# Performance work log

Measured on AMD Instinct MI355X. Metric: run time of the kernel, lower is better.

The kernel has to match this reference:

```python
import jax, jax.numpy as jnp
import numpy as np

B, N, V, H, Z = 2048, 32, 10, 256, 64


def setup_inputs() -> dict:
    key = jax.random.key(0)
    ks = jax.random.split(key, 14)
    # strictly upper-triangular random DAG adjacency (topological order = vertex index)
    p = jax.random.uniform(ks[0], (B, N, N))
    tri = jnp.triu(jnp.ones((N, N), jnp.float32), k=1)
    adj = (p < 0.12).astype(jnp.float32) * tri
    node_types = jax.random.randint(ks[1], (B, N), 0, V).astype(jnp.int32)
    s = 0.05
    return dict(
        adj=adj,
        node_types=node_types,
        w_ih=jax.random.normal(ks[2], (V, 3 * H), jnp.float32) * s,
        w_hh=jax.random.normal(ks[3], (H, 3 * H), jnp.float32) * s,
        b_ih=jax.random.normal(ks[4], (3 * H,), jnp.float32) * s,
        b_hh=jax.random.normal(ks[5], (3 * H,), jnp.float32) * s,
        w_gate=jax.random.normal(ks[6], (H, H), jnp.float32) * s,
        b_gate=jax.random.normal(ks[7], (H,), jnp.float32) * s,
        w_map=jax.random.normal(ks[8], (H, H), jnp.float32) * s,
        w_mu=jax.random.normal(ks[9], (H, Z), jnp.float32) * s,
        b_mu=jax.random.normal(ks[10], (Z,), jnp.float32) * s,
        w_std=jax.random.normal(ks[11], (H, Z), jnp.float32) * s,
        b_std=jax.random.normal(ks[12], (Z,), jnp.float32) * s,
    )


def _gru_cell(x, h, w_ih, w_hh, b_ih, b_hh):
    # torch GRUCell math; weights stored [in, 3H]
    gi = x @ w_ih + b_ih  # [B, 3H]
    gh = h @ w_hh + b_hh
    i_r, i_z, i_n = jnp.split(gi, 3, axis=-1)
    h_r, h_z, h_n = jnp.split(gh, 3, axis=-1)
    r = jax.nn.sigmoid(i_r + h_r)
    z = jax.nn.sigmoid(i_z + h_z)
    n = jnp.tanh(i_n + r * h_n)
    return (1.0 - z) * n + z * h


def reference(adj, node_types, w_ih, w_hh, b_ih, b_hh, w_gate, b_gate, w_map,
              w_mu, b_mu, w_std, b_std):
    x_all = jax.nn.one_hot(node_types, V, dtype=adj.dtype)  # [B, N, V]
    hidden0 = jnp.zeros((B, N, H), adj.dtype)
    adj_cols = jnp.transpose(adj, (2, 0, 1))  # [N, B, N]; col v = predecessor mask of v
    x_seq = jnp.transpose(x_all, (1, 0, 2))   # [N, B, V]

    def step(hidden, inps):
        col, x, v = inps
        # gate(h_pred) * map(h_pred), summed over predecessors. map has no bias,
        # so non-predecessor (zero-masked) rows contribute exactly zero, matching
        # the padded-gather formulation in the original code.
        gm = jax.nn.sigmoid(hidden @ w_gate + b_gate) * (hidden @ w_map)  # [B, N, H]
        agg = jnp.einsum('bn,bnh->bh', col, gm)  # [B, H]; zero for v=0 (no preds)
        h_new = _gru_cell(x, agg, w_ih, w_hh, b_ih, b_hh)  # [B, H]
        hidden = jax.lax.dynamic_update_slice(hidden, h_new[:, None, :], (0, v, 0))
        return hidden, None

    hidden, _ = jax.lax.scan(step, hidden0, (adj_cols, x_seq, jnp.arange(N)))
    hg = hidden[:, -1, :]  # graph state = last vertex hidden
    mu = hg @ w_mu + b_mu
    sigma = hg @ w_std + b_std
    return (mu, sigma)
```

## Files before the change

### kernel.cpp

```cpp
#include <hip/hip_runtime.h>


#define BB 2048
#define NN 32
#define VV 10
#define HH 256
#define ZZ 64
#define BT 8
#define KC 8
#define NT1 48
#define NT2 32
#define WHH_ELEMS (NT1 * KC * 64 * 8)
#define WGM_ELEMS (NT2 * KC * 64 * 8)
#define GM_BYTE_OFF ((WHH_ELEMS + WGM_ELEMS) * 2)
#define SLAB_ELEMS (BT * NN * HH)
#define SLAB_BYTES (SLAB_ELEMS * 2)

typedef __attribute__((ext_vector_type(8))) short frag8;
typedef __attribute__((ext_vector_type(4))) float facc4;
typedef __attribute__((ext_vector_type(4))) unsigned short us4;

__device__ __forceinline__ float bf2f(unsigned short u) {
    unsigned int x = ((unsigned int)u) << 16;
    return __builtin_bit_cast(float, x);
}
__device__ __forceinline__ unsigned short f2bf(float f) {
    unsigned int x = __builtin_bit_cast(unsigned int, f);
    x += 0x7FFFu + ((x >> 16) & 1u);
    return (unsigned short)(x >> 16);
}
__device__ __forceinline__ float sigm(float x) { return 1.0f / (1.0f + __expf(-x)); }
__device__ __forceinline__ float ldv(const float* p, size_t i) { return p[i]; }
__device__ __forceinline__ float ldv(const unsigned short* p, size_t i) { return bf2f(p[i]); }
__device__ __forceinline__ void stv(float* p, size_t i, float v) { p[i] = v; }
__device__ __forceinline__ void stv(unsigned short* p, size_t i, float v) { p[i] = f2bf(v); }
__device__ __forceinline__ us4 ntld4(const unsigned short* p) {
    return __builtin_nontemporal_load((const us4*)p);
}
__device__ __forceinline__ void ntst(unsigned short* p, unsigned short v) {
    __builtin_nontemporal_store(v, p);
}

__global__ void detect_dtype(const unsigned short* __restrict__ w, int* flag) {
    __shared__ int zc, bc;
    if (threadIdx.x == 0) { zc = 0; bc = 0; }
    __syncthreads();
    int z = 0, b = 0;
    for (int i = threadIdx.x; i < 2048; i += 256) {
        unsigned short lo = w[2 * i];
        if (lo == 0) z++;
        unsigned e = (lo >> 7) & 0xFFu;
        if (e >= 0x86u) b++;
    }
    atomicAdd(&zc, z); atomicAdd(&bc, b);
    __syncthreads();
    if (threadIdx.x == 0) *flag = (bc > 0 || zc > 512) ? 1 : 0;
}

template <typename T>
__global__ void repack_weights(const T* __restrict__ w_hh,
                               const T* __restrict__ w_gate,
                               const T* __restrict__ w_map,
                               unsigned short* __restrict__ whh_p,
                               unsigned short* __restrict__ wgm_p,
                               const int* __restrict__ flag, int want) {
    if (*flag != want) return;
    int t = blockIdx.x * blockDim.x + threadIdx.x;
    int lane = t & 63;
    int frag = t >> 6;
    int kbase = (lane >> 4) * 8;
    if (frag < NT1 * KC) {
        int jt = frag / KC, kc = frag % KC;
        int col = jt * 16 + (lane & 15);
        unsigned short* dst = whh_p + ((size_t)frag * 64 + lane) * 8;
        #pragma unroll
        for (int j = 0; j < 8; ++j)
            dst[j] = f2bf(ldv(w_hh, (size_t)(kc * 32 + kbase + j) * 768 + col));
    } else if (frag < (NT1 + NT2) * KC) {
        int f2 = frag - NT1 * KC;
        int jt = f2 / KC, kc = f2 % KC;
        int col = jt * 16 + (lane & 15);
        unsigned short* dst = wgm_p + ((size_t)f2 * 64 + lane) * 8;
        #pragma unroll
        for (int j = 0; j < 8; ++j) {
            int k = kc * 32 + kbase + j;
            dst[j] = f2bf((col < HH) ? ldv(w_gate, (size_t)k * HH + col)
                                     : ldv(w_map, (size_t)k * HH + (col - HH)));
        }
    }
}

template <typename T>
__global__ __launch_bounds__(1024, 4) void vae_main(
    const T* __restrict__ adj,
    const int* __restrict__ ntypes,
    const T* __restrict__ w_ih,
    const T* __restrict__ b_ih,
    const T* __restrict__ b_hh,
    const T* __restrict__ b_gate,
    const T* __restrict__ w_mu,
    const T* __restrict__ b_mu,
    const T* __restrict__ w_std,
    const T* __restrict__ b_std,
    const unsigned short* __restrict__ whh_p,
    const unsigned short* __restrict__ wgm_p,
    unsigned short* __restrict__ gm_base,
    T* __restrict__ out,
    int b_start,
    const int* __restrict__ flag, int want)
{
    if (*flag != want) return;

    __shared__ __align__(16) float agg[BT][HH];
    __shared__ __align__(16) unsigned short aggbf[16][264];
    __shared__ __align__(16) unsigned short hnew[16][264];
    __shared__ unsigned int  amask[BT][NN];
    __shared__ int           ntva[BT][NN];
    __shared__ __align__(16) unsigned short wihL[VV * 776];
    __shared__ __align__(16) float bihL[768], bhhL[768], bgL[HH];

    const int tid  = threadIdx.x;
    const int lane = tid & 63;
    const int w    = tid >> 6;
    const int b0   = b_start + blockIdx.x * BT;

    unsigned short* gms = gm_base + (size_t)blockIdx.x * SLAB_ELEMS;

    const frag8* whh8 = (const frag8*)whh_p;
    const frag8* wgm8 = (const frag8*)wgm_p;

    for (int i = 8 * 264 + tid; i < 16 * 264; i += 1024) {
        ((unsigned short*)aggbf)[i] = 0;
        ((unsigned short*)hnew)[i]  = 0;
    }
    if (tid < 256) {
        int bi = tid >> 5, vv = tid & 31;
        unsigned m = 0;
        for (int n = 0; n < NN; ++n)
            if (ldv(adj, ((size_t)(b0 + bi) * NN + n) * NN + vv) != 0.0f) m |= (1u << n);
        amask[bi][vv] = m;
    } else if (tid < 512) {
        int idx = tid - 256;
        int bi = idx >> 5, vv = idx & 31;
        ntva[bi][vv] = ntypes[(b0 + bi) * NN + vv];
    }
    for (int i = tid; i < VV * 768; i += 1024) {
        int r = i / 768, c = i - r * 768;
        wihL[r * 776 + c] = f2bf(ldv(w_ih, (size_t)i));
    }
    for (int i = tid; i < 768; i += 1024) { bihL[i] = ldv(b_ih, i); bhhL[i] = ldv(b_hh, i); }
    if (tid < HH) bgL[tid] = ldv(b_gate, tid);
    __syncthreads();

    for (int v = 0; v < NN; ++v) {
        if (w < BT) {
            const int bi = w;
            const int h4 = lane * 4;
            unsigned m = amask[bi][v];
            float a0 = 0.f, a1 = 0.f, a2 = 0.f, a3 = 0.f;
            const unsigned short* rb = gms + (size_t)bi * NN * HH + h4;
            while (m) {
                int n = __builtin_ctz(m); m &= m - 1;
                us4 g = ntld4(rb + (size_t)n * HH);
                a0 += bf2f(g.x); a1 += bf2f(g.y); a2 += bf2f(g.z); a3 += bf2f(g.w);
            }
            *(float4*)&agg[bi][h4] = make_float4(a0, a1, a2, a3);
            ushort4 ab; ab.x = f2bf(a0); ab.y = f2bf(a1); ab.z = f2bf(a2); ab.w = f2bf(a3);
            *(ushort4*)&aggbf[bi][h4] = ab;
        }
        __syncthreads();

        {
            frag8 afrag[KC];
            #pragma unroll
            for (int kc = 0; kc < KC; ++kc)
                afrag[kc] = *(const frag8*)&aggbf[lane & 15][kc * 32 + (lane >> 4) * 8];

            const int t = w;
            facc4 aR = {0.f, 0.f, 0.f, 0.f};
            facc4 aZ = {0.f, 0.f, 0.f, 0.f};
            facc4 aN = {0.f, 0.f, 0.f, 0.f};
            const frag8* pR = whh8 + (size_t)(t     ) * (KC * 64) + lane;
            const frag8* pZ = whh8 + (size_t)(t + 16) * (KC * 64) + lane;
            const frag8* pN = whh8 + (size_t)(t + 32) * (KC * 64) + lane;
            #pragma unroll
            for (int kc = 0; kc < KC; ++kc) {
                aR = __builtin_amdgcn_mfma_f32_16x16x32_bf16(afrag[kc], pR[kc * 64], aR, 0, 0, 0);
                aZ = __builtin_amdgcn_mfma_f32_16x16x32_bf16(afrag[kc], pZ[kc * 64], aZ, 0, 0, 0);
                aN = __builtin_amdgcn_mfma_f32_16x16x32_bf16(afrag[kc], pN[kc * 64], aN, 0, 0, 0);
            }
            const int col = t * 16 + (lane & 15);
            const int q = lane >> 4;
            if (q < 2) {
                const float bir  = bihL[col],       bhr = bhhL[col];
                const float biz  = bihL[col + 256], bhz = bhhL[col + 256];
                const float bin_ = bihL[col + 512], bhn = bhhL[col + 512];
                #pragma unroll
                for (int i = 0; i < 4; ++i) {
                    const int bi = 4 * q + i;
                    const int ty = ntva[bi][v] * 776;
                    const float xr = bf2f(wihL[ty + col]);
                    const float xz = bf2f(wihL[ty + col + 256]);
                    const float xn = bf2f(wihL[ty + col + 512]);
                    const float r = sigm(xr + bir + aR[i] + bhr);
                    const float z = sigm(xz + biz + aZ[i] + bhz);
                    const float n = tanhf(xn + bin_ + r * (aN[i] + bhn));
                    const float h = (1.f - z) * n + z * agg[bi][col];
                    hnew[bi][col] = f2bf(h);
                }
            }
        }
        __syncthreads();

        {
            frag8 hfrag[KC];
            #pragma unroll
            for (int kc = 0; kc < KC; ++kc)
                hfrag[kc] = *(const frag8*)&hnew[lane & 15][kc * 32 + (lane >> 4) * 8];

            const int t = w;
            facc4 aG = {0.f, 0.f, 0.f, 0.f};
            facc4 aM = {0.f, 0.f, 0.f, 0.f};
            const frag8* pG = wgm8 + (size_t)(t     ) * (KC * 64) + lane;
            const frag8* pM = wgm8 + (size_t)(t + 16) * (KC * 64) + lane;
            #pragma unroll
            for (int kc = 0; kc < KC; ++kc) {
                aG = __builtin_amdgcn_mfma_f32_16x16x32_bf16(hfrag[kc], pG[kc * 64], aG, 0, 0, 0);
                aM = __builtin_amdgcn_mfma_f32_16x16x32_bf16(hfrag[kc], pM[kc * 64], aM, 0, 0, 0);
            }
            const int col = t * 16 + (lane & 15);
            const int q = lane >> 4;
            if (q < 2) {
                const float bg = bgL[col];
                #pragma unroll
                for (int i = 0; i < 4; ++i) {
                    const int bi = 4 * q + i;
                    const float gv = sigm(aG[i] + bg) * aM[i];
                    ntst(gms + (size_t)(bi * NN + v) * HH + col, f2bf(gv));
                }
            }
        }
        __syncthreads();
    }

    {
        const int bi = w >> 1, half = w & 1, z = lane;
        float am = 0.f, as = 0.f;
        const int h0 = half * 128;
        #pragma unroll 4
        for (int h = h0; h < h0 + 128; ++h) {
            const float hv = bf2f(hnew[bi][h]);
            am += hv * ldv(w_mu, (size_t)h * ZZ + z);
            as += hv * ldv(w_std, (size_t)h * ZZ + z);
        }
        agg[bi][half * 64 + z]       = am;
        agg[bi][128 + half * 64 + z] = as;
    }
    __syncthreads();
    if (w < BT) {
        const int bi = w, z = lane;
        const float am = agg[bi][z] + agg[bi][64 + z] + ldv(b_mu, z);
        const float as = agg[bi][128 + z] + agg[bi][192 + z] + ldv(b_std, z);
        stv(out, (size_t)(b0 + bi) * ZZ + z, am);
        stv(out, (size_t)BB * ZZ + (size_t)(b0 + bi) * ZZ + z, as);
    }
}

extern "C" void kernel_launch(void* const* d_in, const int* in_sizes, int n_in,
                              void* d_out, int out_size, void* d_ws, size_t ws_size,
                              hipStream_t stream)
{
    unsigned short* whh_p = (unsigned short*)d_ws;
    unsigned short* wgm_p = whh_p + WHH_ELEMS;
    unsigned short* gm_base = wgm_p + WGM_ELEMS;

    size_t flag_off = (ws_size >= 8) ? ((ws_size - 4) & ~(size_t)3) : 0;
    int* flag = (int*)((char*)d_ws + flag_off);

    long long avail = (long long)flag_off - (long long)GM_BYTE_OFF;
    int cb = (int)(avail / SLAB_BYTES);
    if (cb < 1) cb = 1;
    if (cb > BB / BT) cb = BB / BT;

    detect_dtype<<<dim3(1), 256, 0, stream>>>((const unsigned short*)d_in[2], flag);

    repack_weights<float><<<dim3(160), 256, 0, stream>>>(
        (const float*)d_in[3], (const float*)d_in[6], (const float*)d_in[8],
        whh_p, wgm_p, flag, 1);
    repack_weights<unsigned short><<<dim3(160), 256, 0, stream>>>(
        (const unsigned short*)d_in[3], (const unsigned short*)d_in[6],
        (const unsigned short*)d_in[8], whh_p, wgm_p, flag, 0);

    const int nblk = BB / BT;
    for (int blk0 = 0; blk0 < nblk; blk0 += cb) {
        int g = nblk - blk0; if (g > cb) g = cb;
        vae_main<float><<<dim3(g), 1024, 0, stream>>>(
            (const float*)d_in[0], (const int*)d_in[1], (const float*)d_in[2],
            (const float*)d_in[4], (const float*)d_in[5], (const float*)d_in[7],
            (const float*)d_in[9], (const float*)d_in[10], (const float*)d_in[11],
            (const float*)d_in[12],
            whh_p, wgm_p, gm_base, (float*)d_out, blk0 * BT, flag, 1);
        vae_main<unsigned short><<<dim3(g), 1024, 0, stream>>>(
            (const unsigned short*)d_in[0], (const int*)d_in[1],
            (const unsigned short*)d_in[2], (const unsigned short*)d_in[4],
            (const unsigned short*)d_in[5], (const unsigned short*)d_in[7],
            (const unsigned short*)d_in[9], (const unsigned short*)d_in[10],
            (const unsigned short*)d_in[11], (const unsigned short*)d_in[12],
            whh_p, wgm_p, gm_base, (unsigned short*)d_out, blk0 * BT, flag, 0);
    }
}
```

Measured before the change: 580.5 us.

## Stage gate*map rows in LDS and write back coalesced; keep gate weights in registers

Instead of each thread issuing scattered 2-byte nontemporal stores of the gate*map row to the global slab, the row is written to a shared-memory buffer. Spare waves then flush it to global memory with 16-byte stores during the next step's aggregation. The immediately preceding vertex's contribution is read straight from LDS rather than from global memory. The gate weight fragments are also preloaded into registers once, removing repeated global loads in the inner MFMA loop, at the cost of extra VGPR pressure and another LDS buffer.

```diff
diff --git a/kernel.cpp b/kernel.cpp
--- a/kernel.cpp
+++ b/kernel.cpp
@@ -19,6 +19,7 @@
 typedef __attribute__((ext_vector_type(8))) short frag8;
 typedef __attribute__((ext_vector_type(4))) float facc4;
 typedef __attribute__((ext_vector_type(4))) unsigned short us4;
+typedef __attribute__((ext_vector_type(8))) unsigned short us8;
 
 __device__ __forceinline__ float bf2f(unsigned short u) {
     unsigned int x = ((unsigned int)u) << 16;
@@ -37,8 +38,8 @@
 __device__ __forceinline__ us4 ntld4(const unsigned short* p) {
     return __builtin_nontemporal_load((const us4*)p);
 }
-__device__ __forceinline__ void ntst(unsigned short* p, unsigned short v) {
-    __builtin_nontemporal_store(v, p);
+__device__ __forceinline__ void ntst16(unsigned short* p, us8 v) {
+    __builtin_nontemporal_store(v, (us8*)p);
 }
 
 __global__ void detect_dtype(const unsigned short* __restrict__ w, int* flag) {
@@ -114,6 +115,7 @@
     __shared__ __align__(16) float agg[BT][HH];
     __shared__ __align__(16) unsigned short aggbf[16][264];
     __shared__ __align__(16) unsigned short hnew[16][264];
+    __shared__ __align__(16) unsigned short gmrow[BT][HH];
     __shared__ unsigned int  amask[BT][NN];
     __shared__ int           ntva[BT][NN];
     __shared__ __align__(16) unsigned short wihL[VV * 776];
@@ -150,13 +152,21 @@
     }
     for (int i = tid; i < 768; i += 1024) { bihL[i] = ldv(b_ih, i); bhhL[i] = ldv(b_hh, i); }
     if (tid < HH) bgL[tid] = ldv(b_gate, tid);
+
+    frag8 wG[KC];
+    {
+        const frag8* pG = wgm8 + (size_t)w * (KC * 64) + lane;
+        #pragma unroll
+        for (int kc = 0; kc < KC; ++kc) wG[kc] = pG[kc * 64];
+    }
     __syncthreads();
 
     for (int v = 0; v < NN; ++v) {
         if (w < BT) {
             const int bi = w;
             const int h4 = lane * 4;
-            unsigned m = amask[bi][v];
+            unsigned m0 = amask[bi][v];
+            unsigned m  = (v > 0) ? (m0 & ~(1u << (v - 1))) : m0;
             float a0 = 0.f, a1 = 0.f, a2 = 0.f, a3 = 0.f;
             const unsigned short* rb = gms + (size_t)bi * NN * HH + h4;
             while (m) {
@@ -164,9 +174,19 @@
                 us4 g = ntld4(rb + (size_t)n * HH);
                 a0 += bf2f(g.x); a1 += bf2f(g.y); a2 += bf2f(g.z); a3 += bf2f(g.w);
             }
+            if (v > 0 && ((m0 >> (v - 1)) & 1u)) {
+                const unsigned short* gr = &gmrow[bi][h4];
+                a0 += bf2f(gr[0]); a1 += bf2f(gr[1]);
+                a2 += bf2f(gr[2]); a3 += bf2f(gr[3]);
+            }
             *(float4*)&agg[bi][h4] = make_float4(a0, a1, a2, a3);
             ushort4 ab; ab.x = f2bf(a0); ab.y = f2bf(a1); ab.z = f2bf(a2); ab.w = f2bf(a3);
             *(ushort4*)&aggbf[bi][h4] = ab;
+        } else if (w < 12 && v > 0) {
+            const int bi = (w - 8) * 2 + (lane >> 5);
+            const int c8 = (lane & 31) * 8;
+            us8 val = *(const us8*)&gmrow[bi][c8];
+            ntst16(gms + ((size_t)bi * NN + (v - 1)) * HH + c8, val);
         }
         __syncthreads();
 
@@ -221,11 +241,10 @@
             const int t = w;
             facc4 aG = {0.f, 0.f, 0.f, 0.f};
             facc4 aM = {0.f, 0.f, 0.f, 0.f};
-            const frag8* pG = wgm8 + (size_t)(t     ) * (KC * 64) + lane;
             const frag8* pM = wgm8 + (size_t)(t + 16) * (KC * 64) + lane;
             #pragma unroll
             for (int kc = 0; kc < KC; ++kc) {
-                aG = __builtin_amdgcn_mfma_f32_16x16x32_bf16(hfrag[kc], pG[kc * 64], aG, 0, 0, 0);
+                aG = __builtin_amdgcn_mfma_f32_16x16x32_bf16(hfrag[kc], wG[kc], aG, 0, 0, 0);
                 aM = __builtin_amdgcn_mfma_f32_16x16x32_bf16(hfrag[kc], pM[kc * 64], aM, 0, 0, 0);
             }
             const int col = t * 16 + (lane & 15);
@@ -235,8 +254,7 @@
                 #pragma unroll
                 for (int i = 0; i < 4; ++i) {
                     const int bi = 4 * q + i;
-                    const float gv = sigm(aG[i] + bg) * aM[i];
-                    ntst(gms + (size_t)(bi * NN + v) * HH + col, f2bf(gv));
+                    gmrow[bi][col] = f2bf(sigm(aG[i] + bg) * aM[i]);
                 }
             }
         }
```

Result: faster. 559.0 us (-3.7%).

## Keep per-block gate*map history in LDS instead of global workspace slab

Applied to the files above, without the earlier changes.

Moves the per-graph gm history (8 graphs x 32 nodes x 256 bf16, 128KB) from a global workspace slab into dynamic shared memory, so the per-step aggregation reads and writes stay on-chip. This also removes the chunked multi-launch loop. To make room, it shrinks the padded aggbf/hnew buffers, stores biases as bf16, and drops the LDS copy of w_ih in favour of direct global reads. It also keeps the R and G weight fragments in registers across steps. The large LDS footprint allows only one block per CU and adds register pressure, but it removes the global memory round-trips that sat on the serial dependency chain.

```diff
diff --git a/kernel.cpp b/kernel.cpp
--- a/kernel.cpp
+++ b/kernel.cpp
@@ -12,13 +12,10 @@
 #define NT2 32
 #define WHH_ELEMS (NT1 * KC * 64 * 8)
 #define WGM_ELEMS (NT2 * KC * 64 * 8)
-#define GM_BYTE_OFF ((WHH_ELEMS + WGM_ELEMS) * 2)
-#define SLAB_ELEMS (BT * NN * HH)
-#define SLAB_BYTES (SLAB_ELEMS * 2)
+#define DYN_LDS_BYTES (BT * NN * HH * 2)
 
 typedef __attribute__((ext_vector_type(8))) short frag8;
 typedef __attribute__((ext_vector_type(4))) float facc4;
-typedef __attribute__((ext_vector_type(4))) unsigned short us4;
 
 __device__ __forceinline__ float bf2f(unsigned short u) {
     unsigned int x = ((unsigned int)u) << 16;
@@ -34,12 +31,6 @@
 __device__ __forceinline__ float ldv(const unsigned short* p, size_t i) { return bf2f(p[i]); }
 __device__ __forceinline__ void stv(float* p, size_t i, float v) { p[i] = v; }
 __device__ __forceinline__ void stv(unsigned short* p, size_t i, float v) { p[i] = f2bf(v); }
-__device__ __forceinline__ us4 ntld4(const unsigned short* p) {
-    return __builtin_nontemporal_load((const us4*)p);
-}
-__device__ __forceinline__ void ntst(unsigned short* p, unsigned short v) {
-    __builtin_nontemporal_store(v, p);
-}
 
 __global__ void detect_dtype(const unsigned short* __restrict__ w, int* flag) {
     __shared__ int zc, bc;
@@ -104,35 +95,29 @@
     const T* __restrict__ b_std,
     const unsigned short* __restrict__ whh_p,
     const unsigned short* __restrict__ wgm_p,
-    unsigned short* __restrict__ gm_base,
     T* __restrict__ out,
-    int b_start,
     const int* __restrict__ flag, int want)
 {
     if (*flag != want) return;
 
+    extern __shared__ __align__(16) char dyn_lds[];
+    unsigned short* gmS = (unsigned short*)dyn_lds;
+
     __shared__ __align__(16) float agg[BT][HH];
-    __shared__ __align__(16) unsigned short aggbf[16][264];
-    __shared__ __align__(16) unsigned short hnew[16][264];
+    __shared__ __align__(16) unsigned short aggbf[BT][264];
+    __shared__ __align__(16) unsigned short hnew[BT][264];
     __shared__ unsigned int  amask[BT][NN];
     __shared__ int           ntva[BT][NN];
-    __shared__ __align__(16) unsigned short wihL[VV * 776];
-    __shared__ __align__(16) float bihL[768], bhhL[768], bgL[HH];
+    __shared__ unsigned short bihL[768], bhhL[768], bgL[HH];
 
     const int tid  = threadIdx.x;
     const int lane = tid & 63;
     const int w    = tid >> 6;
-    const int b0   = b_start + blockIdx.x * BT;
-
-    unsigned short* gms = gm_base + (size_t)blockIdx.x * SLAB_ELEMS;
+    const int b0   = blockIdx.x * BT;
 
     const frag8* whh8 = (const frag8*)whh_p;
     const frag8* wgm8 = (const frag8*)wgm_p;
 
-    for (int i = 8 * 264 + tid; i < 16 * 264; i += 1024) {
-        ((unsigned short*)aggbf)[i] = 0;
-        ((unsigned short*)hnew)[i]  = 0;
-    }
     if (tid < 256) {
         int bi = tid >> 5, vv = tid & 31;
         unsigned m = 0;
@@ -144,26 +129,45 @@
         int bi = idx >> 5, vv = idx & 31;
         ntva[bi][vv] = ntypes[(b0 + bi) * NN + vv];
     }
-    for (int i = tid; i < VV * 768; i += 1024) {
-        int r = i / 768, c = i - r * 768;
-        wihL[r * 776 + c] = f2bf(ldv(w_ih, (size_t)i));
-    }
-    for (int i = tid; i < 768; i += 1024) { bihL[i] = ldv(b_ih, i); bhhL[i] = ldv(b_hh, i); }
-    if (tid < HH) bgL[tid] = ldv(b_gate, tid);
+    for (int i = tid; i < 768; i += 1024) {
+        bihL[i] = f2bf(ldv(b_ih, i));
+        bhhL[i] = f2bf(ldv(b_hh, i));
+    }
+    if (tid < HH) bgL[tid] = f2bf(ldv(b_gate, tid));
+
+    frag8 wR[KC], wG[KC];
+    {
+        const frag8* pR = whh8 + (size_t)w * (KC * 64) + lane;
+        const frag8* pG = wgm8 + (size_t)w * (KC * 64) + lane;
+        #pragma unroll
+        for (int kc = 0; kc < KC; ++kc) { wR[kc] = pR[kc * 64]; wG[kc] = pG[kc * 64]; }
+    }
     __syncthreads();
+
+    const int arow  = lane & 15;
+    const int acol0 = (lane >> 4) * 8;
 
     for (int v = 0; v < NN; ++v) {
         if (w < BT) {
             const int bi = w;
             const int h4 = lane * 4;
+            const unsigned short* rb = gmS + (size_t)(bi * NN) * HH + h4;
             unsigned m = amask[bi][v];
             float a0 = 0.f, a1 = 0.f, a2 = 0.f, a3 = 0.f;
-            const unsigned short* rb = gms + (size_t)bi * NN * HH + h4;
+            float c0 = 0.f, c1 = 0.f, c2 = 0.f, c3 = 0.f;
             while (m) {
-                int n = __builtin_ctz(m); m &= m - 1;
-                us4 g = ntld4(rb + (size_t)n * HH);
-                a0 += bf2f(g.x); a1 += bf2f(g.y); a2 += bf2f(g.z); a3 += bf2f(g.w);
-            }
+                int n0 = __builtin_ctz(m); m &= m - 1;
+                const ushort4 g0 = *(const ushort4*)(rb + n0 * HH);
+                if (m) {
+                    int n1 = __builtin_ctz(m); m &= m - 1;
+                    const ushort4 g1 = *(const ushort4*)(rb + n1 * HH);
+                    c0 += bf2f(g1.x); c1 += bf2f(g1.y);
+                    c2 += bf2f(g1.z); c3 += bf2f(g1.w);
+                }
+                a0 += bf2f(g0.x); a1 += bf2f(g0.y);
+                a2 += bf2f(g0.z); a3 += bf2f(g0.w);
+            }
+            a0 += c0; a1 += c1; a2 += c2; a3 += c3;
             *(float4*)&agg[bi][h4] = make_float4(a0, a1, a2, a3);
             ushort4 ab; ab.x = f2bf(a0); ab.y = f2bf(a1); ab.z = f2bf(a2); ab.w = f2bf(a3);
             *(ushort4*)&aggbf[bi][h4] = ab;
@@ -172,36 +176,40 @@
 
         {
             frag8 afrag[KC];
-            #pragma unroll
-            for (int kc = 0; kc < KC; ++kc)
-                afrag[kc] = *(const frag8*)&aggbf[lane & 15][kc * 32 + (lane >> 4) * 8];
+            if (arow < BT) {
+                #pragma unroll
+                for (int kc = 0; kc < KC; ++kc)
+                    afrag[kc] = *(const frag8*)&aggbf[arow][kc * 32 + acol0];
+            } else {
+                #pragma unroll
+                for (int kc = 0; kc < KC; ++kc) afrag[kc] = frag8{};
+            }
 
             const int t = w;
             facc4 aR = {0.f, 0.f, 0.f, 0.f};
             facc4 aZ = {0.f, 0.f, 0.f, 0.f};
             facc4 aN = {0.f, 0.f, 0.f, 0.f};
-            const frag8* pR = whh8 + (size_t)(t     ) * (KC * 64) + lane;
             const frag8* pZ = whh8 + (size_t)(t + 16) * (KC * 64) + lane;
             const frag8* pN = whh8 + (size_t)(t + 32) * (KC * 64) + lane;
             #pragma unroll
             for (int kc = 0; kc < KC; ++kc) {
-                aR = __builtin_amdgcn_mfma_f32_16x16x32_bf16(afrag[kc], pR[kc * 64], aR, 0, 0, 0);
+                aR = __builtin_amdgcn_mfma_f32_16x16x32_bf16(afrag[kc], wR[kc], aR, 0, 0, 0);
                 aZ = __builtin_amdgcn_mfma_f32_16x16x32_bf16(afrag[kc], pZ[kc * 64], aZ, 0, 0, 0);
                 aN = __builtin_amdgcn_mfma_f32_16x16x32_bf16(afrag[kc], pN[kc * 64], aN, 0, 0, 0);
             }
             const int col = t * 16 + (lane & 15);
             const int q = lane >> 4;
             if (q < 2) {
-                const float bir  = bihL[col],       bhr = bhhL[col];
-                const float biz  = bihL[col + 256], bhz = bhhL[col + 256];
-                const float bin_ = bihL[col + 512], bhn = bhhL[col + 512];
+                const float bir  = bf2f(bihL[col]),       bhr = bf2f(bhhL[col]);
+                const float biz  = bf2f(bihL[col + 256]), bhz = bf2f(bhhL[col + 256]);
+                const float bin_ = bf2f(bihL[col + 512]), bhn = bf2f(bhhL[col + 512]);
                 #pragma unroll
                 for (int i = 0; i < 4; ++i) {
                     const int bi = 4 * q + i;
-                    const int ty = ntva[bi][v] * 776;
-                    const float xr = bf2f(wihL[ty + col]);
-                    const float xz = bf2f(wihL[ty + col + 256]);
-                    const float xn = bf2f(wihL[ty + col + 512]);
+                    const size_t ty = (size_t)ntva[bi][v] * 768;
+                    const float xr = ldv(w_ih, ty + col);
+                    const float xz = ldv(w_ih, ty + col + 256);
+                    const float xn = ldv(w_ih, ty + col + 512);
                     const float r = sigm(xr + bir + aR[i] + bhr);
                     const float z = sigm(xz + biz + aZ[i] + bhz);
                     const float n = tanhf(xn + bin_ + r * (aN[i] + bhn));
@@ -214,29 +222,32 @@
 
         {
             frag8 hfrag[KC];
-            #pragma unroll
-            for (int kc = 0; kc < KC; ++kc)
-                hfrag[kc] = *(const frag8*)&hnew[lane & 15][kc * 32 + (lane >> 4) * 8];
+            if (arow < BT) {
+                #pragma unroll
+                for (int kc = 0; kc < KC; ++kc)
+                    hfrag[kc] = *(const frag8*)&hnew[arow][kc * 32 + acol0];
+            } else {
+                #pragma unroll
+                for (int kc = 0; kc < KC; ++kc) hfrag[kc] = frag8{};
+            }
 
             const int t = w;
             facc4 aG = {0.f, 0.f, 0.f, 0.f};
             facc4 aM = {0.f, 0.f, 0.f, 0.f};
-            const frag8* pG = wgm8 + (size_t)(t     ) * (KC * 64) + lane;
             const frag8* pM = wgm8 + (size_t)(t + 16) * (KC * 64) + lane;
             #pragma unroll
             for (int kc = 0; kc < KC; ++kc) {
-                aG = __builtin_amdgcn_mfma_f32_16x16x32_bf16(hfrag[kc], pG[kc * 64], aG, 0, 0, 0);
+                aG = __builtin_amdgcn_mfma_f32_16x16x32_bf16(hfrag[kc], wG[kc], aG, 0, 0, 0);
                 aM = __builtin_amdgcn_mfma_f32_16x16x32_bf16(hfrag[kc], pM[kc * 64], aM, 0, 0, 0);
             }
             const int col = t * 16 + (lane & 15);
             const int q = lane >> 4;
             if (q < 2) {
-                const float bg = bgL[col];
+                const float bg = bf2f(bgL[col]);
                 #pragma unroll
                 for (int i = 0; i < 4; ++i) {
                     const int bi = 4 * q + i;
-                    const float gv = sigm(aG[i] + bg) * aM[i];
-                    ntst(gms + (size_t)(bi * NN + v) * HH + col, f2bf(gv));
+                    gmS[(size_t)(bi * NN + v) * HH + col] = f2bf(sigm(aG[i] + bg) * aM[i]);
                 }
             }
         }
@@ -272,15 +283,14 @@
 {
     unsigned short* whh_p = (unsigned short*)d_ws;
     unsigned short* wgm_p = whh_p + WHH_ELEMS;
-    unsigned short* gm_base = wgm_p + WGM_ELEMS;
 
     size_t flag_off = (ws_size >= 8) ? ((ws_size - 4) & ~(size_t)3) : 0;
     int* flag = (int*)((char*)d_ws + flag_off);
 
-    long long avail = (long long)flag_off - (long long)GM_BYTE_OFF;
-    int cb = (int)(avail / SLAB_BYTES);
-    if (cb < 1) cb = 1;
-    if (cb > BB / BT) cb = BB / BT;
+    (void)hipFuncSetAttribute(reinterpret_cast<const void*>(&vae_main<float>),
+                              hipFuncAttributeMaxDynamicSharedMemorySize, DYN_LDS_BYTES);
+    (void)hipFuncSetAttribute(reinterpret_cast<const void*>(&vae_main<unsigned short>),
+                              hipFuncAttributeMaxDynamicSharedMemorySize, DYN_LDS_BYTES);
 
     detect_dtype<<<dim3(1), 256, 0, stream>>>((const unsigned short*)d_in[2], flag);
 
@@ -291,21 +301,16 @@
         (const unsigned short*)d_in[3], (const unsigned short*)d_in[6],
         (const unsigned short*)d_in[8], whh_p, wgm_p, flag, 0);
 
-    const int nblk = BB / BT;
-    for (int blk0 = 0; blk0 < nblk; blk0 += cb) {
-        int g = nblk - blk0; if (g > cb) g = cb;
-        vae_main<float><<<dim3(g), 1024, 0, stream>>>(
-            (const float*)d_in[0], (const int*)d_in[1], (const float*)d_in[2],
-            (const float*)d_in[4], (const float*)d_in[5], (const float*)d_in[7],
-            (const float*)d_in[9], (const float*)d_in[10], (const float*)d_in[11],
-            (const float*)d_in[12],
-            whh_p, wgm_p, gm_base, (float*)d_out, blk0 * BT, flag, 1);
-        vae_main<unsigned short><<<dim3(g), 1024, 0, stream>>>(
-            (const unsigned short*)d_in[0], (const int*)d_in[1],
-            (const unsigned short*)d_in[2], (const unsigned short*)d_in[4],
-            (const unsigned short*)d_in[5], (const unsigned short*)d_in[7],
-            (const unsigned short*)d_in[9], (const unsigned short*)d_in[10],
-            (const unsigned short*)d_in[11], (const unsigned short*)d_in[12],
-            whh_p, wgm_p, gm_base, (unsigned short*)d_out, blk0 * BT, flag, 0);
-    }
-}
+    vae_main<float><<<dim3(BB / BT), 1024, DYN_LDS_BYTES, stream>>>(
+        (const float*)d_in[0], (const int*)d_in[1], (const float*)d_in[2],
+        (const float*)d_in[4], (const float*)d_in[5], (const float*)d_in[7],
+        (const float*)d_in[9], (const float*)d_in[10], (const float*)d_in[11],
+        (const float*)d_in[12], whh_p, wgm_p, (float*)d_out, flag, 1);
+    vae_main<unsigned short><<<dim3(BB / BT), 1024, DYN_LDS_BYTES, stream>>>(
+        (const unsigned short*)d_in[0], (const int*)d_in[1],
+        (const unsigned short*)d_in[2], (const unsigned short*)d_in[4],
+        (const unsigned short*)d_in[5], (const unsigned short*)d_in[7],
+        (const unsigned short*)d_in[9], (const unsigned short*)d_in[10],
+        (const unsigned short*)d_in[11], (const unsigned short*)d_in[12],
+        whh_p, wgm_p, (unsigned short*)d_out, flag, 0);
+}
```

Result: slower. 601.1 us (+3.6%).
